# Performance work log

Measured on AMD Instinct MI355X. Metric: run time of the kernel, lower is better.

The kernel has to match this reference:

```python
import jax, jax.numpy as jnp
from jax import lax
import numpy as np

H, W = 4096, 4096
KH, KW = 15, 15


def setup_inputs() -> dict:
    key = jax.random.key(0)
    kx, kw = jax.random.split(key)
    X = jax.random.normal(kx, (H, W), dtype=jnp.float32)
    weight = jax.random.uniform(kw, (KH, KW), dtype=jnp.float32)
    bias = jnp.zeros((1,), dtype=jnp.float32)
    return {"X": X, "weight": weight, "bias": bias}


def reference(X, weight, bias):
    # Valid 2D cross-correlation (no kernel flip), matching corr2d.
    # lax.conv_general_dilated performs cross-correlation by default.
    out = lax.conv_general_dilated(
        X[None, None, :, :],            # NCHW: [1, 1, H, W]
        weight[None, None, :, :],       # OIHW: [1, 1, KH, KW]
        window_strides=(1, 1),
        padding="VALID",
    )
    return out[0, 0] + bias[0]          # [H-KH+1, W-KW+1]
```

## Files before the change

kernel.cpp:

```cpp
#include <hip/hip_runtime.h>
#include <hip/hip_bf16.h>

#define H_IN 4096
#define W_IN 4096
#define KH 15
#define KW 15
#define OH (H_IN - KH + 1)
#define OW (W_IN - KW + 1)

#define BM 64
#define BN 128
#define NJ (BN / 16)
#define SROWS (BM + KH - 1)
#define SCOLS 144
#define SSTR  152
#define SCH4 36
#define STAGE_N (SROWS * SCH4)

typedef __attribute__((ext_vector_type(8))) short short8;
typedef __attribute__((ext_vector_type(4))) float f32x4;

__device__ __forceinline__ ushort f2bf(float f) {
    __hip_bfloat16 h = __float2bfloat16(f);
    return __builtin_bit_cast(ushort, h);
}

__global__ __launch_bounds__(256)
void build_wfrags(const float* __restrict__ Wt, ushort* __restrict__ Bw)
{
    int idx = blockIdx.x * 256 + threadIdx.x;
    if (idx < KH * 64) {
        int kh = idx >> 6, l = idx & 63;
        int j = l & 15, k0 = (l >> 4) * 8;
        union { ushort u[8]; uint4 v; } t;
#pragma unroll
        for (int u = 0; u < 8; ++u) {
            int kw = k0 + u - j;
            t.u[u] = f2bf((kw >= 0 && kw < KW) ? Wt[kh * KW + kw] : 0.0f);
        }
        *reinterpret_cast<uint4*>(&Bw[idx * 8]) = t.v;
    }
}

__global__ __launch_bounds__(256, 5)
void conv2d_mfma_bf16(const float* __restrict__ X,
                      const ushort* __restrict__ Bw,
                      const float* __restrict__ Bias,
                      float* __restrict__ Out)
{
    __shared__ ushort s_x[SROWS * SSTR];

    const int tid = threadIdx.x;
    const int l = tid & 63;
    const int w = tid >> 6;
    const int ox0 = blockIdx.x * BN;
    const int oy0 = blockIdx.y * BM;

    const bool xint = (ox0 + SCOLS <= W_IN);
    for (int i = tid; i < STAGE_N; i += 256) {
        int r  = i / SCH4;
        int c4 = i % SCH4;
        int gy = min(oy0 + r, H_IN - 1);
        const float* rp = X + (size_t)gy * W_IN;
        int gx = ox0 + c4 * 4;
        float4 v;
        if (xint) {
            v = *reinterpret_cast<const float4*>(rp + gx);
        } else {
            v.x = rp[min(gx + 0, W_IN - 1)];
            v.y = rp[min(gx + 1, W_IN - 1)];
            v.z = rp[min(gx + 2, W_IN - 1)];
            v.w = rp[min(gx + 3, W_IN - 1)];
        }
        uint2 pk;
        pk.x = (uint32_t)f2bf(v.x) | ((uint32_t)f2bf(v.y) << 16);
        pk.y = (uint32_t)f2bf(v.z) | ((uint32_t)f2bf(v.w) << 16);
        *reinterpret_cast<uint2*>(&s_x[r * SSTR + c4 * 4]) = pk;
    }
    __syncthreads();

    const ushort* const abase = &s_x[(w * 16 + (l & 15)) * SSTR + (l >> 4) * 8];
    const ushort* const bbase = Bw + l * 8;

    f32x4 acc[NJ];
#pragma unroll
    for (int j = 0; j < NJ; ++j) acc[j] = (f32x4){0.f, 0.f, 0.f, 0.f};

#pragma unroll
    for (int kh = 0; kh < KH; ++kh) {
        short8 bf = *reinterpret_cast<const short8*>(bbase + kh * 64 * 8);
        const ushort* arow = abase + kh * SSTR;
#pragma unroll
        for (int j = 0; j < NJ; ++j) {
            short8 a = *reinterpret_cast<const short8*>(arow + j * 16);
            acc[j] = __builtin_amdgcn_mfma_f32_16x16x32_bf16(a, bf, acc[j], 0, 0, 0);
        }
    }

    const float b = Bias[0];
    const int orow0 = oy0 + w * 16 + (l >> 4) * 4;
    const int ocol  = ox0 + (l & 15);
    if (oy0 + BM <= OH && ox0 + BN <= OW) {
        float* op0 = &Out[(size_t)orow0 * OW + ocol];
#pragma unroll
        for (int j = 0; j < NJ; ++j) {
#pragma unroll
            for (int r = 0; r < 4; ++r)
                op0[(size_t)r * OW + j * 16] = acc[j][r] + b;
        }
    } else {
#pragma unroll
        for (int j = 0; j < NJ; ++j) {
            int oc = ocol + j * 16;
            if (oc < OW) {
#pragma unroll
                for (int r = 0; r < 4; ++r) {
                    int orow = orow0 + r;
                    if (orow < OH)
                        Out[(size_t)orow * OW + oc] = acc[j][r] + b;
                }
            }
        }
    }
}

extern "C" void kernel_launch(void* const* d_in, const int* in_sizes, int n_in,
                              void* d_out, int out_size, void* d_ws, size_t ws_size,
                              hipStream_t stream)
{
    const float* X    = (const float*)d_in[0];
    const float* Wt   = (const float*)d_in[1];
    const float* Bias = (const float*)d_in[2];
    float* Out        = (float*)d_out;
    ushort* Bw        = (ushort*)d_ws;

    hipLaunchKernelGGL(build_wfrags, dim3((KH * 64 + 255) / 256), dim3(256), 0, stream,
                       Wt, Bw);

    dim3 grid((OW + BN - 1) / BN,
              (OH + BM - 1) / BM);
    dim3 block(256);
    hipLaunchKernelGGL(conv2d_mfma_bf16, grid, block, 0, stream, X, Bw, Bias, Out);
}
```

Measured before the change: 51.52 us.

## Pre-convert input to bf16 and stage tiles via direct global-to-LDS loads

Adds a separate pass that converts the whole fp32 input to bf16 in the workspace. The conv kernel then fills shared memory with global_load_lds 16-byte DMA instead of per-thread loads, converts and LDS stores, and keeps all weight fragments in registers before the MFMA loop. This is meant to cut halo load traffic (bf16 tiles are half-size) and staging instruction overhead. In exchange it adds a full extra read and write of the input, and a fallback path that runs when the workspace is too small.

Result: faster. 50.36 us (-2.3%).

```diff
diff --git a/kernel.cpp b/kernel.cpp
--- a/kernel.cpp
+++ b/kernel.cpp
@@ -12,10 +12,13 @@
 #define BN 128
 #define NJ (BN / 16)
 #define SROWS (BM + KH - 1)
-#define SCOLS 144
+#define SGROW 19
 #define SSTR  152
-#define SCH4 36
-#define STAGE_N (SROWS * SCH4)
+#define DMAGR 1536
+
+#define XBF_ELEMS ((size_t)H_IN * W_IN)
+#define XBF_PAD   ((XBF_ELEMS + 4096) * 2)
+#define WS_NEED   (XBF_PAD + (size_t)KH * 64 * 8 * 2)
 
 typedef __attribute__((ext_vector_type(8))) short short8;
 typedef __attribute__((ext_vector_type(4))) float f32x4;
@@ -23,6 +26,26 @@
 __device__ __forceinline__ ushort f2bf(float f) {
     __hip_bfloat16 h = __float2bfloat16(f);
     return __builtin_bit_cast(ushort, h);
+}
+__device__ __forceinline__ uint32_t pk2(float a, float b) {
+    return (uint32_t)f2bf(a) | ((uint32_t)f2bf(b) << 16);
+}
+__device__ __forceinline__ void gload_lds16(const void* g, void* l) {
+    __builtin_amdgcn_global_load_lds(
+        (const __attribute__((address_space(1))) void*)g,
+        (__attribute__((address_space(3))) void*)l, 16, 0, 0);
+}
+
+__global__ __launch_bounds__(256, 8)
+void convert_bf16(const float* __restrict__ X, ushort* __restrict__ Xb)
+{
+    size_t i8 = ((size_t)blockIdx.x * 256 + threadIdx.x) * 8;
+    float4 a = *reinterpret_cast<const float4*>(X + i8);
+    float4 b = *reinterpret_cast<const float4*>(X + i8 + 4);
+    uint4 pk;
+    pk.x = pk2(a.x, a.y); pk.y = pk2(a.z, a.w);
+    pk.z = pk2(b.x, b.y); pk.w = pk2(b.z, b.w);
+    *reinterpret_cast<uint4*>(Xb + i8) = pk;
 }
 
 __global__ __launch_bounds__(256)
@@ -42,13 +65,13 @@
     }
 }
 
-__global__ __launch_bounds__(256, 5)
-void conv2d_mfma_bf16(const float* __restrict__ X,
-                      const ushort* __restrict__ Bw,
-                      const float* __restrict__ Bias,
-                      float* __restrict__ Out)
-{
-    __shared__ ushort s_x[SROWS * SSTR];
+__global__ __launch_bounds__(256, 4)
+void conv2d_mfma_dma(const ushort* __restrict__ Xb,
+                     const ushort* __restrict__ Bw,
+                     const float* __restrict__ Bias,
+                     float* __restrict__ Out)
+{
+    __shared__ ushort s_x[DMAGR * 8];
 
     const int tid = threadIdx.x;
     const int l = tid & 63;
@@ -56,31 +79,25 @@
     const int ox0 = blockIdx.x * BN;
     const int oy0 = blockIdx.y * BM;
 
-    const bool xint = (ox0 + SCOLS <= W_IN);
-    for (int i = tid; i < STAGE_N; i += 256) {
-        int r  = i / SCH4;
-        int c4 = i % SCH4;
+#pragma unroll
+    for (int k = 0; k < 6; ++k) {
+        int i = tid + 256 * k;
+        int r = i / SGROW;
+        int g = i - r * SGROW;
         int gy = min(oy0 + r, H_IN - 1);
-        const float* rp = X + (size_t)gy * W_IN;
-        int gx = ox0 + c4 * 4;
-        float4 v;
-        if (xint) {
-            v = *reinterpret_cast<const float4*>(rp + gx);
-        } else {
-            v.x = rp[min(gx + 0, W_IN - 1)];
-            v.y = rp[min(gx + 1, W_IN - 1)];
-            v.z = rp[min(gx + 2, W_IN - 1)];
-            v.w = rp[min(gx + 3, W_IN - 1)];
-        }
-        uint2 pk;
-        pk.x = (uint32_t)f2bf(v.x) | ((uint32_t)f2bf(v.y) << 16);
-        pk.y = (uint32_t)f2bf(v.z) | ((uint32_t)f2bf(v.w) << 16);
-        *reinterpret_cast<uint2*>(&s_x[r * SSTR + c4 * 4]) = pk;
+        const ushort* src = Xb + (size_t)gy * W_IN + (ox0 + g * 8);
+        gload_lds16(src, (char*)s_x + (k * 4 + w) * 1024);
     }
     __syncthreads();
 
+    const ushort* const bbase = Bw + l * 8;
+    short8 bfr[KH];
+#pragma unroll
+    for (int kh = 0; kh < KH; ++kh)
+        bfr[kh] = *reinterpret_cast<const short8*>(bbase + kh * 64 * 8);
+    __builtin_amdgcn_sched_barrier(0);
+
     const ushort* const abase = &s_x[(w * 16 + (l & 15)) * SSTR + (l >> 4) * 8];
-    const ushort* const bbase = Bw + l * 8;
 
     f32x4 acc[NJ];
 #pragma unroll
@@ -88,12 +105,11 @@
 
 #pragma unroll
     for (int kh = 0; kh < KH; ++kh) {
-        short8 bf = *reinterpret_cast<const short8*>(bbase + kh * 64 * 8);
         const ushort* arow = abase + kh * SSTR;
 #pragma unroll
         for (int j = 0; j < NJ; ++j) {
             short8 a = *reinterpret_cast<const short8*>(arow + j * 16);
-            acc[j] = __builtin_amdgcn_mfma_f32_16x16x32_bf16(a, bf, acc[j], 0, 0, 0);
+            acc[j] = __builtin_amdgcn_mfma_f32_16x16x32_bf16(a, bfr[kh], acc[j], 0, 0, 0);
         }
     }
 
@@ -124,6 +140,83 @@
     }
 }
 
+__global__ __launch_bounds__(256, 4)
+void conv2d_fallback(const float* __restrict__ X,
+                     const float* __restrict__ Wt,
+                     const float* __restrict__ Bias,
+                     float* __restrict__ Out)
+{
+    __shared__ ushort s_w[KH * 64 * 8];
+    __shared__ ushort s_x[SROWS * SSTR];
+
+    const int tid = threadIdx.x;
+    const int l = tid & 63;
+    const int w = tid >> 6;
+    const int ox0 = blockIdx.x * BN;
+    const int oy0 = blockIdx.y * BM;
+    const bool xint = (ox0 + 144 <= W_IN);
+
+    for (int idx = tid; idx < KH * 64; idx += 256) {
+        int kh = idx >> 6, ll = idx & 63;
+        int j = ll & 15, k0 = (ll >> 4) * 8;
+        union { ushort u[8]; uint4 q; } t;
+#pragma unroll
+        for (int u = 0; u < 8; ++u) {
+            int kw = k0 + u - j;
+            t.u[u] = f2bf((kw >= 0 && kw < KW) ? Wt[kh * KW + kw] : 0.0f);
+        }
+        *reinterpret_cast<uint4*>(&s_w[idx * 8]) = t.q;
+    }
+
+    for (int i = tid; i < SROWS * 36; i += 256) {
+        int r = i / 36, c4 = i % 36;
+        int gy = min(oy0 + r, H_IN - 1);
+        const float* rp = X + (size_t)gy * W_IN;
+        int gx = ox0 + c4 * 4;
+        float4 v;
+        if (xint) v = *reinterpret_cast<const float4*>(rp + gx);
+        else {
+            v.x = rp[min(gx + 0, W_IN - 1)];
+            v.y = rp[min(gx + 1, W_IN - 1)];
+            v.z = rp[min(gx + 2, W_IN - 1)];
+            v.w = rp[min(gx + 3, W_IN - 1)];
+        }
+        uint2 pk; pk.x = pk2(v.x, v.y); pk.y = pk2(v.z, v.w);
+        *reinterpret_cast<uint2*>(&s_x[r * SSTR + c4 * 4]) = pk;
+    }
+    __syncthreads();
+
+    const ushort* const abase = &s_x[(w * 16 + (l & 15)) * SSTR + (l >> 4) * 8];
+    const ushort* const bbase = &s_w[l * 8];
+    f32x4 acc[NJ];
+#pragma unroll
+    for (int j = 0; j < NJ; ++j) acc[j] = (f32x4){0.f, 0.f, 0.f, 0.f};
+#pragma unroll
+    for (int kh = 0; kh < KH; ++kh) {
+        short8 bf = *reinterpret_cast<const short8*>(bbase + kh * 64 * 8);
+        const ushort* arow = abase + kh * SSTR;
+#pragma unroll
+        for (int j = 0; j < NJ; ++j) {
+            short8 a = *reinterpret_cast<const short8*>(arow + j * 16);
+            acc[j] = __builtin_amdgcn_mfma_f32_16x16x32_bf16(a, bf, acc[j], 0, 0, 0);
+        }
+    }
+    const float b = Bias[0];
+    const int orow0 = oy0 + w * 16 + (l >> 4) * 4;
+    const int ocol  = ox0 + (l & 15);
+#pragma unroll
+    for (int j = 0; j < NJ; ++j) {
+        int oc = ocol + j * 16;
+        if (oc < OW) {
+#pragma unroll
+            for (int r = 0; r < 4; ++r) {
+                int orow = orow0 + r;
+                if (orow < OH) Out[(size_t)orow * OW + oc] = acc[j][r] + b;
+            }
+        }
+    }
+}
+
 extern "C" void kernel_launch(void* const* d_in, const int* in_sizes, int n_in,
                               void* d_out, int out_size, void* d_ws, size_t ws_size,
                               hipStream_t stream)
@@ -132,13 +225,21 @@
     const float* Wt   = (const float*)d_in[1];
     const float* Bias = (const float*)d_in[2];
     float* Out        = (float*)d_out;
-    ushort* Bw        = (ushort*)d_ws;
-
-    hipLaunchKernelGGL(build_wfrags, dim3((KH * 64 + 255) / 256), dim3(256), 0, stream,
-                       Wt, Bw);
-
-    dim3 grid((OW + BN - 1) / BN,
-              (OH + BM - 1) / BM);
-    dim3 block(256);
-    hipLaunchKernelGGL(conv2d_mfma_bf16, grid, block, 0, stream, X, Bw, Bias, Out);
-}
+
+    if (ws_size >= WS_NEED) {
+        ushort* Xb = (ushort*)d_ws;
+        ushort* Bw = (ushort*)((char*)d_ws + XBF_PAD);
+
+        hipLaunchKernelGGL(convert_bf16, dim3(XBF_ELEMS / 8 / 256), dim3(256), 0, stream,
+                           X, Xb);
+        hipLaunchKernelGGL(build_wfrags, dim3((KH * 64 + 255) / 256), dim3(256), 0, stream,
+                           Wt, Bw);
+        dim3 grid((OW + BN - 1) / BN, (OH + BM - 1) / BM);
+        hipLaunchKernelGGL(conv2d_mfma_dma, grid, dim3(256), 0, stream,
+                           Xb, Bw, Bias, Out);
+    } else {
+        dim3 grid((OW + BN - 1) / BN, (OH + BM - 1) / BM);
+        hipLaunchKernelGGL(conv2d_fallback, grid, dim3(256), 0, stream,
+                           X, Wt, Bias, Out);
+    }
+}
```
